# Kernel optimization log

Hardware: AMD Instinct MI355X
Metric: run time of the kernel (lower is better)

Reference implementation:

```python
import jax, jax.numpy as jnp
import numpy as np

WINDOW = 32


def _dilate(mask, iters=5):
    # scipy binary_dilation with default cross structure, `iters` iterations
    m = mask.copy()
    for _ in range(iters):
        d = m.copy()
        d[1:, :] |= m[:-1, :]
        d[:-1, :] |= m[1:, :]
        d[:, 1:] |= m[:, :-1]
        d[:, :-1] |= m[:, 1:]
        m = d
    return m


def _label8(mask):
    # skimage measure.label, default 8-connectivity, via min-label propagation
    h, w = mask.shape
    lab = np.where(mask, np.arange(1, mask.size + 1, dtype=np.int64).reshape(h, w), 0)
    BIG = mask.size + 2
    while True:
        p = np.pad(np.where(mask, lab, BIG), 1, constant_values=BIG)
        m = np.full((h, w), BIG, dtype=np.int64)
        for dy in (-1, 0, 1):
            for dx in (-1, 0, 1):
                m = np.minimum(m, p[1 + dy:1 + dy + h, 1 + dx:1 + dx + w])
        new = np.where(mask, m, 0)
        if np.array_equal(new, lab):
            break
        lab = new
    u = np.unique(lab)
    out = np.searchsorted(u, lab)
    if u[0] != 0:
        out = out + 1
    return out


def _malis(seg_flat, e1, e2, costs, pos):
    # MALIS edge weights: Kruskal on descending affinities with union-find;
    # pos=True counts same-(nonzero)-label pairs merged by each edge,
    # pos=False counts cross-label pairs between labeled nodes.
    n = seg_flat.size
    parent = np.arange(n)
    cnt = [dict() for _ in range(n)]
    for i in range(n):
        s = int(seg_flat[i])
        if s != 0:
            cnt[i][s] = 1
    w = np.zeros(costs.shape[0], np.float32)

    def find(x):
        r = x
        while parent[r] != r:
            r = parent[r]
        while parent[x] != r:
            parent[x], x = r, parent[x]
        return r

    order = np.argsort(-costs, kind='stable')
    for ei in order:
        ra, rb = find(int(e1[ei])), find(int(e2[ei]))
        if ra == rb:
            continue
        ca, cb = cnt[ra], cnt[rb]
        small, large = (ca, cb) if len(ca) <= len(cb) else (cb, ca)
        same = 0
        for kk, v in small.items():
            same += v * large.get(kk, 0)
        if pos:
            w[ei] = same
        else:
            sa = sum(ca.values())
            sb = sum(cb.values())
            w[ei] = sa * sb - same
        parent[rb] = ra
        for kk, v in cb.items():
            ca[kk] = ca.get(kk, 0) + v
        cnt[rb] = None
    return w


def compute_malis_weights(pred_np, target_np):
    B, C, H, W = pred_np.shape
    wn_full = np.zeros(pred_np.shape, np.float32)
    wp_full = np.zeros(pred_np.shape, np.float32)
    win = WINDOW
    idx = np.arange(win * win).reshape(win, win)
    e1 = np.concatenate([idx[:, :-1].ravel(), idx[:-1, :].ravel()])
    e2 = np.concatenate([idx[:, 1:].ravel(), idx[1:, :].ravel()])
    for k in range(H // win):
        for j in range(W // win):
            p = pred_np[:, :, k * win:(k + 1) * win, j * win:(j + 1) * win]
            t = target_np[:, :, k * win:(k + 1) * win, j * win:(j + 1) * win]
            costs = np.concatenate([
                (p[:, :, :, :-1] + p[:, :, :, 1:]).reshape(B, -1),
                (p[:, :, :-1, :] + p[:, :, 1:, :]).reshape(B, -1)], axis=1).astype(np.float32)
            gtc = np.concatenate([
                (t[:, :, :, :-1] + t[:, :, :, 1:]).reshape(B, -1),
                (t[:, :, :-1, :] + t[:, :, 1:, :]).reshape(B, -1)], axis=1).astype(np.float32)
            costs_n = costs.copy()
            costs_p = costs.copy()
            costs_n[gtc > 20] = 20
            costs_p[gtc < 10] = 0
            gtc = np.minimum(gtc, 20)
            for i in range(B):
                sg = _label8(_dilate(t[i, 0] == 0, 5) == 0)
                en = _malis(sg.ravel(), e1, e2, costs_n[i], False)
                ep = _malis(sg.ravel(), e1, e2, costs_p[i], True)
                sn = en.sum()
                if sn > 0:
                    en = en / sn
                sp = ep.sum()
                if sp > 0:
                    ep = ep / sp
                en[gtc[i] >= 10] = 0
                ep[gtc[i] < 20] = 0
                for ew, out in ((en, wn_full), (ep, wp_full)):
                    wh, wv = np.split(ew, 2)
                    wh = wh.reshape(win, win - 1)
                    wv = wv.reshape(win - 1, win)
                    nodes = np.zeros((win, win), np.float32)
                    nodes[:, :-1] += wh
                    nodes[:, 1:] += wh
                    nodes[:-1, :] += wv
                    nodes[1:, :] += wv
                    out[i, 0, k * win:(k + 1) * win, j * win:(j + 1) * win] = nodes
    return wn_full, wp_full


def setup_inputs() -> dict:
    key = jax.random.key(0)
    k1, k2 = jax.random.split(key)
    pred = jax.random.uniform(k1, (2, 1, 256, 256), jnp.float32) * 20.0
    target = jax.random.randint(k2, (2, 1, 256, 256), 0, 26).astype(jnp.float32)
    return {"pred": pred, "target": target, "malis_lr": 1.0, "malis_lr_pos": 1.0}


def reference(pred, target, malis_lr, malis_lr_pos):
    # weights are computed from detached values (CPU graph algorithm), constants wrt autodiff
    wn, wp = compute_malis_weights(np.asarray(pred), np.asarray(target))
    wn = jnp.asarray(wn, jnp.float32)
    wp = jnp.asarray(wp, jnp.float32)
    loss = malis_lr * jnp.square(pred) * wn + malis_lr_pos * jnp.square(20.0 - pred) * wp
    return loss.sum()
```

## Files before the change

### kernel.cpp

```cpp
#include <hip/hip_runtime.h>
#include <cstdint>

#define NPIX  1024
#define NH    992
#define NEDGE 1984
#define NSORT 2048
#define NGRP  31
#define HFS   4300
#define POOLN (NPIX + 2*HFS)

typedef unsigned long long u64;
typedef unsigned int u32;

static __device__ __forceinline__ u64 packRoot(int sL,int off,int len,int cap){
    return (u64)(u32)(sL & 0x7FF) | ((u64)(u32)(off & 0x3FFF) << 11) |
           ((u64)(u32)(len & 0x7FF) << 25) | ((u64)(u32)(cap & 0x7FF) << 36);
}
#define R_SL(R)  ((int)((R) & 0x7FF))
#define R_OFF(R) ((int)(((R)>>11) & 0x3FFF))
#define R_LEN(R) ((int)(((R)>>25) & 0x7FF))
#define R_CAP(R) ((int)(((R)>>36) & 0x7FF))
#define EMASK 0x3FFFFFFu

static __device__ __forceinline__ int rdl(int v, int l){ return __builtin_amdgcn_readlane(v, l); }

static __device__ __forceinline__ u64 sxor64(u64 v, int m){
    u32 lo = (u32)__shfl_xor((int)(v & 0xFFFFFFFFull), m, 64);
    u32 hi = (u32)__shfl_xor((int)(v >> 32), m, 64);
    return ((u64)hi << 32) | lo;
}

static __device__ __forceinline__ void edgeAB(int e, int &a, int &b){
    if (e < NH) { int r = (int)((unsigned)e / 31u); a = e + r; b = a + 1; }
    else        { a = e - NH; b = a + 32; }
}

#define CE(x, y, up) { u64 _a=(x), _b=(y); bool _lt=(_a<_b); \
    u64 _mn=_lt?_a:_b, _mx=_lt?_b:_a; (x)=(up)?_mn:_mx; (y)=(up)?_mx:_mn; }
#define CEX(x, xm, keepmin) { u64 _p=sxor64((x),(xm)); bool _lt=((x)<_p); \
    u64 _mn=_lt?(x):_p, _mx=_lt?_p:(x); (x)=(keepmin)?_mn:_mx; }

static __device__ __forceinline__ int wredi(int v){
    #pragma unroll
    for (int o = 32; o > 0; o >>= 1) v += __shfl_xor(v, o, 64);
    return v;
}
static __device__ __forceinline__ float wredf(float v){
    #pragma unroll
    for (int o = 32; o > 0; o >>= 1) v += __shfl_xor(v, o, 64);
    return v;
}

__global__ __launch_bounds__(128) void malis_kernel(
    const float* __restrict__ pred,
    const float* __restrict__ target,
    const float* __restrict__ lr_p,
    const float* __restrict__ lrp_p,
    float* __restrict__ out)
{
    const int tid  = threadIdx.x;
    const int lane = tid & 63;
    const int wv   = tid >> 6;
    const int bid  = blockIdx.x;
    const int bb   = bid >> 6;
    const int win  = bid & 63;
    const int wy   = win >> 3, wx = win & 7;
    const int base = bb * 65536 + (wy * 32) * 256 + wx * 32;

    __shared__ __align__(16) u32 Ks[2][NSORT];
    __shared__ u64   root[2][NPIX];
    __shared__ float predL[NPIX];
    __shared__ float costs[NEDGE];
    __shared__ u32   poolS[2][POOLN];
    __shared__ u32   Q[2][NPIX];
    __shared__ float Qw[2][NPIX];
    __shared__ short seg[NPIX];
    __shared__ short par[2][NPIX];
    __shared__ short H[2][NPIX + 1];
    __shared__ unsigned char tgtL[NPIX];
    __shared__ unsigned char gtcL[NEDGE];
    __shared__ u32   rowmaskL[32];
    __shared__ u32   fgL[32];
    __shared__ unsigned short baseL[33];
    __shared__ int   flags[2];

    u32* runPar = (u32*)poolS;
    unsigned short* labIdRun = (unsigned short*)(runPar + 512);

    for (int j = 0; j < 8; ++j) {
        int i = tid + 128 * j;
        int r = i >> 5, c = i & 31;
        float pv = pred[base + r * 256 + c];
        float tv = target[base + r * 256 + c];
        predL[i] = pv;
        tgtL[i]  = (unsigned char)tv;
        u64 zb = __ballot(tv == 0.0f);
        if (lane == 0) {
            int rr = 4 * j + 2 * wv;
            rowmaskL[rr]     = (u32)zb;
            rowmaskL[rr + 1] = (u32)(zb >> 32);
        }
    }
    if (tid == 0) flags[1] = 0;
    for (int x = tid; x < 512; x += 128) runPar[x] = (u32)x;
    __syncthreads();

    if (tid < 32) {
        u32 m = rowmaskL[tid];
        #pragma unroll
        for (int it = 0; it < 5; ++it) {
            u32 um = __shfl(m, (tid == 0) ? 0 : tid - 1, 64);
            if (tid == 0) um = 0;
            u32 dm = __shfl(m, (tid == 31) ? 31 : tid + 1, 64);
            if (tid == 31) dm = 0;
            m = m | (m << 1) | (m >> 1) | um | dm;
        }
        u32 f = ~m;
        fgL[tid] = f;
        int ns = __popc(f & ~(f << 1));
        int x = ns;
        #pragma unroll
        for (int off = 1; off < 32; off <<= 1) {
            int y = __shfl(x, (tid >= off) ? tid - off : 0, 64);
            if (tid >= off) x += y;
        }
        baseL[tid] = (unsigned short)(x - ns);
        if (tid == 31) baseL[32] = (unsigned short)x;
    }
    __syncthreads();
    const int nRuns = (int)baseL[32];

    for (;;) {
        if (tid == 0) flags[0] = 0;
        __syncthreads();
        bool chg = false;
        for (int j = 0; j < 8; ++j) {
            int i = tid + 128 * j;
            int r = i >> 5, c = i & 31;
            if (r == 0) continue;
            u32 fr = fgL[r];
            if (!((fr >> c) & 1u)) continue;
            u32 fu = fgL[r - 1];
            u32 nb = fu & (u32)((7ull << c) >> 1);
            if (!nb) continue;
            u32 Sr = fr & ~(fr << 1);
            int a = (int)baseL[r] + __popc(Sr & ((2u << c) - 1u)) - 1;
            for (;;) { int p = (int)runPar[a]; if (p == a) break; a = p; }
            u32 Su = fu & ~(fu << 1);
            int bu = (int)baseL[r - 1];
            while (nb) {
                int cc = __ffs((int)nb) - 1; nb &= nb - 1;
                int b = bu + __popc(Su & ((2u << cc) - 1u)) - 1;
                for (;;) { int p = (int)runPar[b]; if (p == b) break; b = p; }
                if (a != b) {
                    int mnr = a < b ? a : b;
                    int mxr = a ^ b ^ mnr;
                    atomicMin(&runPar[mxr], (u32)mnr);
                    chg = true;
                    a = mnr;
                }
            }
        }
        if (chg) flags[0] = 1;
        __syncthreads();
        if (!flags[0]) break;
        for (int x = tid; x < nRuns; x += 128) {
            u32 p = runPar[x];
            runPar[x] = runPar[p];
        }
        __syncthreads();
    }

    for (int x = tid; x < nRuns; x += 128)
        if ((int)runPar[x] == x) labIdRun[x] = (unsigned short)atomicAdd(&flags[1], 1);
    __syncthreads();

    for (int j = 0; j < 8; ++j) {
        int i = tid + 128 * j;
        int r = i >> 5, c = i & 31;
        u32 fr = fgL[r];
        short s = 0;
        if ((fr >> c) & 1u) {
            u32 Sr = fr & ~(fr << 1);
            int x = (int)baseL[r] + __popc(Sr & ((2u << c) - 1u)) - 1;
            for (;;) { int p = (int)runPar[x]; if (p == x) break; x = p; }
            s = (short)((int)labIdRun[x] + 1);
        }
        seg[i] = s;
    }

    for (int e = tid; e < NEDGE; e += 128) {
        int a, b2; edgeAB(e, a, b2);
        costs[e] = predL[a] + predL[b2];
        gtcL[e]  = (unsigned char)(tgtL[a] + tgtL[b2]);
    }
    __syncthreads();

    const int ph = wv;
    u32*   Ks_   = Ks[ph];
    short* par_  = par[ph];
    u64*   root_ = root[ph];
    u32*   pool_ = poolS[ph];
    short* H_    = H[ph];
    u32*   Q_    = Q[ph];
    float* Qw_   = Qw[ph];
    u32*   claim_= (u32*)Qw[ph];

    u64 sk[32];
    #pragma unroll
    for (int r = 0; r < 32; ++r) {
        int e = lane * 32 + r;
        u64 kv = ~0ULL;
        if (e < NEDGE) {
            float cv = costs[e];
            int g = gtcL[e];
            if (ph == 0) { if (g > 20) cv = 20.0f; }
            else         { if (g < 10) cv = 0.0f; }
            kv = (((u64)(~__float_as_uint(cv))) << 32) | (u32)e;
        }
        sk[r] = kv;
    }
    #pragma unroll
    for (int kk2 = 2; kk2 <= 32; kk2 <<= 1) {
        #pragma unroll
        for (int j = kk2 >> 1; j > 0; j >>= 1) {
            #pragma unroll
            for (int r = 0; r < 32; ++r) {
                if ((r & j) == 0) {
                    bool up = (kk2 == 32) ? ((lane & 1) == 0) : ((r & kk2) == 0);
                    CE(sk[r], sk[r | j], up);
                }
            }
        }
    }
    #pragma unroll
    for (int kk2 = 64; kk2 <= 2048; kk2 <<= 1) {
        const bool up = ((lane & (kk2 >> 5)) == 0);
        #pragma unroll
        for (int j = kk2 >> 1; j >= 32; j >>= 1) {
            const int xm = j >> 5;
            const bool keepmin = (((lane & xm) == 0) == up);
            #pragma unroll
            for (int r = 0; r < 32; ++r) { CEX(sk[r], xm, keepmin); }
        }
        #pragma unroll
        for (int j = 16; j > 0; j >>= 1) {
            #pragma unroll
            for (int r = 0; r < 32; ++r) {
                if ((r & j) == 0) { CE(sk[r], sk[r | j], up); }
            }
        }
    }
    #pragma unroll
    for (int r = 0; r < 32; r += 4) {
        uint4 v4;
        v4.x = (u32)sk[r]; v4.y = (u32)sk[r+1]; v4.z = (u32)sk[r+2]; v4.w = (u32)sk[r+3];
        *(uint4*)&Ks_[lane * 32 + r] = v4;
    }

    for (int i = lane; i < NPIX; i += 64) {
        short s2 = seg[i];
        par_[i] = (short)(i | (s2 ? 0x8000 : 0));
        root_[i] = s2 ? ((1ull << 62) | ((u32)(unsigned short)s2 << 16) | 1u) : 0ull;
        H_[i] = 0;
        claim_[i] = ~0u;
    }
    if (lane == 0) H_[NPIX] = 0;
    __builtin_amdgcn_wave_barrier();

    int qn = 0;
    u32 rnd = 1;
    const u64 ltm = (1ull << lane) - 1;
    int curE = (int)Ks_[lane];
    for (int g2 = 0; g2 < NGRP; ++g2) {
        int nextE = (g2 + 1 < NGRP) ? (int)Ks_[(g2 + 1) * 64 + lane] : 0;
        const int myE = curE;
        int ea, eb2; edgeAB(myE, ea, eb2);
        int ra = ea, rb = eb2;
        int laA, laB;
        for (;;) {
            int va = (int)(unsigned short)par_[ra];
            int vb = (int)(unsigned short)par_[rb];
            int pa = va & 0x3FF, pb = vb & 0x3FF;
            bool fa = (pa != ra), fb = (pb != rb);
            if (!fa && !fb) { laA = va >> 15; laB = vb >> 15; break; }
            int ga = (int)(unsigned short)par_[pa];
            int gb = (int)(unsigned short)par_[pb];
            if (fa) { par_[ra] = (short)ga; ra = ga & 0x3FF; }
            if (fb) { par_[rb] = (short)gb; rb = gb & 0x3FF; }
        }
        bool alive = (ra != rb);

        for (;;) {
            if (!__ballot(alive)) break;
            const bool av = alive;
            const u32 tag = ((0x03FFFFFFu - rnd) << 6) | (u32)lane;
            ++rnd;
            int mn = ra < rb ? ra : rb;
            int mx = ra < rb ? rb : ra;
            int winner = (laA == laB) ? mn : (laA ? ra : rb);
            int loser  = (laA == laB) ? mx : (laA ? rb : ra);
            bool wgt = (laA & laB) != 0;
            if (av)        atomicMin(&claim_[loser],  tag);
            if (av && wgt) atomicMin(&claim_[winner], tag);
            bool sel = false;
            if (av) {
                u32 cl = claim_[loser];
                u32 cw = wgt ? claim_[winner] : tag;
                sel = (cl == tag) && (cw == tag);
            }
            u64 wm = __ballot(sel && wgt);
            if (sel && wgt) Q_[qn + __popcll(wm & ltm)] =
                (u32)myE | ((u32)mn << 11) | ((u32)mx << 21);
            qn += (int)__popcll(wm);
            if (sel) par_[loser] = (short)winner;
            if (av) {
                for (;;) {
                    int va = (int)(unsigned short)par_[ra];
                    int vb = (int)(unsigned short)par_[rb];
                    int pa = va & 0x3FF, pb = vb & 0x3FF;
                    bool fa = (pa != ra), fb = (pb != rb);
                    if (!fa && !fb) { laA = va >> 15; laB = vb >> 15; break; }
                    int ga = (int)(unsigned short)par_[pa];
                    int gb = (int)(unsigned short)par_[pb];
                    if (fa) { par_[ra] = (short)ga; ra = ga & 0x3FF; }
                    if (fb) { par_[rb] = (short)gb; rb = gb & 0x3FF; }
                }
                alive = !sel && (ra != rb);
            }
        }
        curE = nextE;
        __builtin_amdgcn_wave_barrier();
    }

    u32 bump = NPIX;
    u32 halfEnd = NPIX + HFS;
    int curHalf = 0;

    auto do_gc = [&]() {
        u32 tgt = (curHalf == 0) ? (u32)(NPIX + HFS) : (u32)NPIX;
        u32 nb = tgt;
        for (int c = 0; c < 16; ++c) {
            int i0 = c * 64 + lane;
            u64 Ri = root_[i0];
            bool live = (Ri != 0) && ((Ri >> 62) == 0);
            u64 rbm = __ballot(live);
            while (rbm) {
                int j = __ffsll(rbm) - 1; rbm &= rbm - 1;
                int r = c * 64 + j;
                u64 R = root_[r];
                int len = R_LEN(R);
                int off = R_OFF(R);
                for (int t = lane; t < len; t += 64) {
                    u32 v2 = pool_[off + t];
                    pool_[nb + t] = v2;
                }
                __builtin_amdgcn_wave_barrier();
                if (lane == 0) root_[r] = packRoot(R_SL(R), (int)nb, len, len);
                nb += (u32)len;
            }
        }
        bump = nb;
        halfEnd = tgt + HFS;
        curHalf ^= 1;
    };

    u32 rec = 0; u64 RA = 0, RB = 0;
    if (qn > 0) {
        rec = Q_[0];
        int A0 = (int)((rec >> 11) & 0x3FF), B0 = (int)((rec >> 21) & 0x3FF);
        RA = root_[A0]; RB = root_[B0];
    }
    for (int q = 0; q < qn; ++q) {
        const int A = (int)((rec >> 11) & 0x3FF);
        const int B = (int)((rec >> 21) & 0x3FF);
        int tA = (int)(RA >> 62), tB = (int)(RB >> 62);
        int same, sLa, sLb;
        u64 newR;

        if (tA == 1 && tB == 1) {
            u32 pa = (u32)RA & EMASK, pb = (u32)RB & EMASK;
            int ca = (int)(pa & 0xFFFF), cb = (int)(pb & 0xFFFF);
            sLa = ca; sLb = cb;
            if ((pa >> 16) == (pb >> 16)) {
                same = ca * cb;
                newR = (1ull << 62) | (u64)(pa + (u32)cb);
            } else {
                same = 0;
                newR = (2ull << 62) | ((u64)pb << 26) | pa;
            }
        } else {
            int lenA = tA ? tA : R_LEN(RA);
            int lenB = tB ? tB : R_LEN(RB);
            if (bump + (u32)(lenA + lenB + 8) > halfEnd) {
                do_gc();
                RA = root_[A]; RB = root_[B];
                tA = (int)(RA >> 62); tB = (int)(RB >> 62);
                lenA = tA ? tA : R_LEN(RA);
                lenB = tB ? tB : R_LEN(RB);
            }
            int offA = 0, capA = 0, offB = 0, capB = 0;
            if (tA == 0) { sLa = R_SL(RA); offA = R_OFF(RA); capA = R_CAP(RA); }
            else {
                u32 a0 = (u32)RA & EMASK, a1 = (u32)(RA >> 26) & EMASK;
                sLa = (int)(a0 & 0xFFFF) + ((tA == 2) ? (int)(a1 & 0xFFFF) : 0);
            }
            if (tB == 0) { sLb = R_SL(RB); offB = R_OFF(RB); capB = R_CAP(RB); }
            else {
                u32 b0 = (u32)RB & EMASK, b1 = (u32)(RB >> 26) & EMASK;
                sLb = (int)(b0 & 0xFFFF) + ((tB == 2) ? (int)(b1 & 0xFFFF) : 0);
            }
            u32 eA = 0, eB = 0;
            if (lenA <= 64) {
                if (tA == 0) { if (lane < lenA) eA = pool_[offA + lane]; }
                else {
                    u32 a0 = (u32)RA & EMASK, a1 = (u32)(RA >> 26) & EMASK;
                    eA = (lane == 0) ? a0 : ((lane == 1 && tA == 2) ? a1 : 0);
                }
            }
            if (lenB <= 64) {
                if (tB == 0) { if (lane < lenB) eB = pool_[offB + lane]; }
                else {
                    u32 b0 = (u32)RB & EMASK, b1 = (u32)(RB >> 26) & EMASK;
                    eB = (lane == 0) ? b0 : ((lane == 1 && tB == 2) ? b1 : 0);
                }
            }
            u32 eS, eL; int lenS, lenL, offS, offL, capL, tS, tL;
            if (lenA <= lenB) { eS=eA; lenS=lenA; offS=offA; tS=tA; eL=eB; lenL=lenB; offL=offB; capL=capB; tL=tB; }
            else              { eS=eB; lenS=lenB; offS=offB; tS=tB; eL=eA; lenL=lenA; offL=offA; capL=capA; tL=tA; }
            int dOff, dLen, dCap;
            same = 0;

            if (lenS + lenL <= 64) {
                dLen = lenL;
                for (int t = 0; t < lenS; ++t) {
                    u32 xs = (u32)rdl((int)eS, t);
                    bool match = (lane < lenL) && ((eL >> 16) == (xs >> 16));
                    u64 mb = __ballot(match);
                    if (mb) {
                        int ml = __ffsll(mb) - 1;
                        same += (int)(xs & 0xFFFF) * ((int)rdl((int)eL, ml) & 0xFFFF);
                        if (match) eL += (xs & 0xFFFF);
                    } else {
                        if (lane == dLen) eL = xs;
                        dLen++;
                    }
                }
                if (dLen <= 2) {
                    u32 m0 = (u32)rdl((int)eL, 0) & EMASK;
                    u32 m1 = (dLen > 1) ? ((u32)rdl((int)eL, 1) & EMASK) : 0u;
                    newR = ((u64)(u32)dLen << 62) | ((u64)m1 << 26) | m0;
                } else {
                    if (tL == 0 && dLen <= capL) { dOff = offL; dCap = capL; }
                    else { dOff = (int)bump; dCap = (dLen + 3) & ~3; bump += (u32)dCap; }
                    if (lane < dLen) pool_[dOff + lane] = eL;
                    newR = packRoot(sLa + sLb, dOff, dLen, dCap);
                }
            } else {
                dOff = (int)bump;
                dCap = (lenL + lenS + 4) & ~3; bump += (u32)dCap;
                if (lenS <= 64) {
                    if (lane < lenS) H_[eS >> 16] = (short)(eS & 0xFFFF);
                } else {
                    for (int j = lane; j < lenS; j += 64) {
                        u32 es = pool_[offS + j];
                        H_[es >> 16] = (short)(es & 0xFFFF);
                    }
                }
                __builtin_amdgcn_wave_barrier();
                int sp = 0;
                for (int j = lane; j < lenL; j += 64) {
                    u32 el = pool_[offL + j];
                    int h = (int)H_[el >> 16];
                    sp += h * (int)(el & 0xFFFF);
                    pool_[dOff + j] = el + (u32)h;
                    if (h) H_[el >> 16] = 0;
                }
                same = wredi(sp);
                __builtin_amdgcn_wave_barrier();
                int baseU = 0;
                if (lenS <= 64) {
                    bool un = (lane < lenS) && (H_[eS >> 16] != 0);
                    u64 ub = __ballot(un);
                    if (un) {
                        int pos = __popcll(ub & ltm);
                        pool_[dOff + lenL + pos] = eS;
                        H_[eS >> 16] = 0;
                    }
                    baseU = (int)__popcll(ub);
                } else {
                    for (int j0 = 0; j0 < lenS; j0 += 64) {
                        int j = j0 + lane;
                        bool un = false; u32 es = 0;
                        if (j < lenS) { es = pool_[offS + j]; un = (H_[es >> 16] != 0); }
                        u64 ub = __ballot(un);
                        if (un) {
                            int pos = __popcll(ub & ltm);
                            pool_[dOff + lenL + baseU + pos] = es;
                            H_[es >> 16] = 0;
                        }
                        baseU += (int)__popcll(ub);
                    }
                }
                dLen = lenL + baseU;
                newR = packRoot(sLa + sLb, dOff, dLen, dCap);
            }
        }

        float w = (float)(ph ? same : (sLa * sLb - same));

        u32 recN = 0; int An = -1, Bn = -1; u64 RAn = 0, RBn = 0;
        if (q + 1 < qn) {
            recN = Q_[q + 1];
            An = (int)((recN >> 11) & 0x3FF);
            Bn = (int)((recN >> 21) & 0x3FF);
            RAn = root_[An]; RBn = root_[Bn];
        }
        if (lane == 0) {
            Qw_[q] = w;
            root_[A] = newR;
            root_[B] = 0;
        }
        __builtin_amdgcn_wave_barrier();
        if (An == A) RAn = newR;
        if (Bn == A) RBn = newR;
        rec = recN; RA = RAn; RB = RBn;
    }

    float s_loc = 0.0f;
    for (int q = lane; q < qn; q += 64) s_loc += Qw_[q];
    const float sn = wredf(s_loc);

    const float scale = ph ? lrp_p[0] : lr_p[0];
    float acc = 0.0f;
    for (int q = lane; q < qn; q += 64) {
        float wv2 = Qw_[q];
        if (wv2 == 0.0f) continue;
        if (sn > 0.0f) wv2 /= sn;
        int me = (int)(Q_[q] & 0x7FF);
        int g = gtcL[me];
        bool zero = ph ? (g < 20) : (g >= 10);
        if (zero) continue;
        int a2, b2; edgeAB(me, a2, b2);
        float pa = predL[a2], pb = predL[b2];
        float fa2, fb2;
        if (ph == 0) { fa2 = pa * pa; fb2 = pb * pb; }
        else { float qa = 20.0f - pa, qb = 20.0f - pb; fa2 = qa * qa; fb2 = qb * qb; }
        acc += scale * wv2 * (fa2 + fb2);
    }
    acc = wredf(acc);
    if (lane == 0) atomicAdd(out, acc);
}

__global__ void zero_out_kernel(float* o)
{
    if (threadIdx.x == 0 && blockIdx.x == 0) o[0] = 0.0f;
}

extern "C" void kernel_launch(void* const* d_in, const int* in_sizes, int n_in,
                              void* d_out, int out_size, void* d_ws, size_t ws_size,
                              hipStream_t stream)
{
    const float* pred   = (const float*)d_in[0];
    const float* target = (const float*)d_in[1];
    const float* lr     = (const float*)d_in[2];
    const float* lrp    = (const float*)d_in[3];
    float* out = (float*)d_out;

    zero_out_kernel<<<1, 64, 0, stream>>>(out);
    malis_kernel<<<128, 128, 0, stream>>>(pred, target, lr, lrp, out);
}
```

Before: 337.2 us.

## Fuse label-histogram merging into the parallel union-find rounds

Folds the serial per-merge label-count processing into the wave-parallel Kruskal claim loop. Each lane whose merge involves small inline roots (one or two labels) computes its weight and updates the roots itself. Only merges that overflow fall back to a serialized per-lane pool path inside the loop. This removes the separate sequential replay over the merge queue, at the cost of a dedicated claim array, more shared memory, and extra divergence and register pressure in the hot loop.

```diff
diff --git a/kernel.cpp b/kernel.cpp
--- a/kernel.cpp
+++ b/kernel.cpp
@@ -72,8 +72,9 @@
     __shared__ float predL[NPIX];
     __shared__ float costs[NEDGE];
     __shared__ u32   poolS[2][POOLN];
-    __shared__ u32   Q[2][NPIX];
+    __shared__ unsigned short Q[2][NPIX];
     __shared__ float Qw[2][NPIX];
+    __shared__ u32   claimS[2][NPIX];
     __shared__ short seg[NPIX];
     __shared__ short par[2][NPIX];
     __shared__ short H[2][NPIX + 1];
@@ -202,9 +203,9 @@
     u64*   root_ = root[ph];
     u32*   pool_ = poolS[ph];
     short* H_    = H[ph];
-    u32*   Q_    = Q[ph];
+    unsigned short* Q_ = Q[ph];
     float* Qw_   = Qw[ph];
-    u32*   claim_= (u32*)Qw[ph];
+    u32*   claim_= claimS[ph];
 
     u64 sk[32];
     #pragma unroll
@@ -268,9 +269,41 @@
     if (lane == 0) H_[NPIX] = 0;
     __builtin_amdgcn_wave_barrier();
 
+    const u64 ltm = (1ull << lane) - 1;
+    u32 bump = NPIX;
+    u32 halfEnd = NPIX + HFS;
+    int curHalf = 0;
+
+    auto do_gc = [&]() {
+        u32 tgt = (curHalf == 0) ? (u32)(NPIX + HFS) : (u32)NPIX;
+        u32 nb = tgt;
+        for (int c = 0; c < 16; ++c) {
+            int i0 = c * 64 + lane;
+            u64 Ri = root_[i0];
+            bool live = (Ri != 0) && ((Ri >> 62) == 0);
+            u64 rbm = __ballot(live);
+            while (rbm) {
+                int j = __ffsll(rbm) - 1; rbm &= rbm - 1;
+                int r = c * 64 + j;
+                u64 R = root_[r];
+                int len = R_LEN(R);
+                int off = R_OFF(R);
+                for (int t = lane; t < len; t += 64) {
+                    u32 v2 = pool_[off + t];
+                    pool_[nb + t] = v2;
+                }
+                __builtin_amdgcn_wave_barrier();
+                if (lane == 0) root_[r] = packRoot(R_SL(R), (int)nb, len, len);
+                nb += (u32)len;
+            }
+        }
+        bump = nb;
+        halfEnd = tgt + HFS;
+        curHalf ^= 1;
+    };
+
     int qn = 0;
     u32 rnd = 1;
-    const u64 ltm = (1ull << lane) - 1;
     int curE = (int)Ks_[lane];
     for (int g2 = 0; g2 < NGRP; ++g2) {
         int nextE = (g2 + 1 < NGRP) ? (int)Ks_[(g2 + 1) * 64 + lane] : 0;
@@ -297,7 +330,7 @@
             const u32 tag = ((0x03FFFFFFu - rnd) << 6) | (u32)lane;
             ++rnd;
             int mn = ra < rb ? ra : rb;
-            int mx = ra < rb ? rb : ra;
+            int mx = ra ^ rb ^ mn;
             int winner = (laA == laB) ? mn : (laA ? ra : rb);
             int loser  = (laA == laB) ? mx : (laA ? rb : ra);
             bool wgt = (laA & laB) != 0;
@@ -310,10 +343,182 @@
                 sel = (cl == tag) && (cw == tag);
             }
             u64 wm = __ballot(sel && wgt);
-            if (sel && wgt) Q_[qn + __popcll(wm & ltm)] =
-                (u32)myE | ((u32)mn << 11) | ((u32)mx << 21);
+            int qidx = qn + (int)__popcll(wm & ltm);
             qn += (int)__popcll(wm);
             if (sel) par_[loser] = (short)winner;
+
+            bool needPool = false;
+            if (sel && wgt) {
+                u64 RW = root_[mn], RL = root_[mx];
+                int tW = (int)(RW >> 62), tL2 = (int)(RL >> 62);
+                if (tW != 0 && tL2 != 0) {
+                    u32 a0 = (u32)RW & EMASK, a1 = (u32)(RW >> 26) & EMASK;
+                    u32 b0 = (u32)RL & EMASK, b1 = (u32)(RL >> 26) & EMASK;
+                    u32 la0 = a0 >> 16, la1 = a1 >> 16;
+                    u32 lb0 = b0 >> 16, lb1 = b1 >> 16;
+                    int ca0 = (int)(a0 & 0xFFFF), ca1 = (int)(a1 & 0xFFFF);
+                    int cb0 = (int)(b0 & 0xFFFF), cb1 = (int)(b1 & 0xFFFF);
+                    int sLa = ca0 + ((tW == 2) ? ca1 : 0);
+                    int sLb = cb0 + ((tL2 == 2) ? cb1 : 0);
+                    int same = 0;
+                    if (lb0 == la0) same += ca0 * cb0;
+                    else if (tW == 2 && lb0 == la1) same += ca1 * cb0;
+                    if (tL2 == 2) {
+                        if (lb1 == la0) same += ca0 * cb1;
+                        else if (tW == 2 && lb1 == la1) same += ca1 * cb1;
+                    }
+                    u32 r0 = a0, r1 = (tW == 2) ? a1 : 0;
+                    int n = tW; bool ovf = false;
+                    if (lb0 == la0) r0 += (u32)cb0;
+                    else if (tW == 2 && lb0 == la1) r1 += (u32)cb0;
+                    else { if (n == 1) { r1 = b0; n = 2; } else ovf = true; }
+                    if (tL2 == 2) {
+                        if (lb1 == la0) r0 += (u32)cb1;
+                        else if (tW == 2 && lb1 == la1) r1 += (u32)cb1;
+                        else { if (n == 1) { r1 = b1; n = 2; } else ovf = true; }
+                    }
+                    if (!ovf) {
+                        root_[mn] = ((u64)(u32)n << 62) | ((u64)r1 << 26) | r0;
+                        root_[mx] = 0;
+                        Qw_[qidx] = (float)(ph ? same : (sLa * sLb - same));
+                        Q_[qidx]  = (unsigned short)myE;
+                    } else needPool = true;
+                } else needPool = true;
+            }
+
+            u64 pm = __ballot(needPool);
+            while (pm) {
+                int f = __ffsll(pm) - 1; pm &= pm - 1;
+                int A  = rdl(mn, f),  B  = rdl(mx, f);
+                int e  = rdl(myE, f), qi = rdl(qidx, f);
+                u64 RA = root_[A], RB = root_[B];
+                int tA = (int)(RA >> 62), tB = (int)(RB >> 62);
+                int lenA = tA ? tA : R_LEN(RA);
+                int lenB = tB ? tB : R_LEN(RB);
+                if (bump + (u32)(lenA + lenB + 8) > halfEnd) {
+                    do_gc();
+                    RA = root_[A]; RB = root_[B];
+                    tA = (int)(RA >> 62); tB = (int)(RB >> 62);
+                    lenA = tA ? tA : R_LEN(RA);
+                    lenB = tB ? tB : R_LEN(RB);
+                }
+                int sLa, sLb;
+                int offA = 0, capA = 0, offB = 0, capB = 0;
+                if (tA == 0) { sLa = R_SL(RA); offA = R_OFF(RA); capA = R_CAP(RA); }
+                else {
+                    u32 a0 = (u32)RA & EMASK, a1 = (u32)(RA >> 26) & EMASK;
+                    sLa = (int)(a0 & 0xFFFF) + ((tA == 2) ? (int)(a1 & 0xFFFF) : 0);
+                }
+                if (tB == 0) { sLb = R_SL(RB); offB = R_OFF(RB); capB = R_CAP(RB); }
+                else {
+                    u32 b0 = (u32)RB & EMASK, b1 = (u32)(RB >> 26) & EMASK;
+                    sLb = (int)(b0 & 0xFFFF) + ((tB == 2) ? (int)(b1 & 0xFFFF) : 0);
+                }
+                u32 eA = 0, eB = 0;
+                if (lenA <= 64) {
+                    if (tA == 0) { if (lane < lenA) eA = pool_[offA + lane]; }
+                    else {
+                        u32 a0 = (u32)RA & EMASK, a1 = (u32)(RA >> 26) & EMASK;
+                        eA = (lane == 0) ? a0 : ((lane == 1 && tA == 2) ? a1 : 0);
+                    }
+                }
+                if (lenB <= 64) {
+                    if (tB == 0) { if (lane < lenB) eB = pool_[offB + lane]; }
+                    else {
+                        u32 b0 = (u32)RB & EMASK, b1 = (u32)(RB >> 26) & EMASK;
+                        eB = (lane == 0) ? b0 : ((lane == 1 && tB == 2) ? b1 : 0);
+                    }
+                }
+                u32 eS, eL; int lenS, lenL, offS, offL, capL, tL;
+                if (lenA <= lenB) { eS=eA; lenS=lenA; offS=offA; eL=eB; lenL=lenB; offL=offB; capL=capB; tL=tB; }
+                else              { eS=eB; lenS=lenB; offS=offB; eL=eA; lenL=lenA; offL=offA; capL=capA; tL=tA; }
+                int dOff, dLen, dCap;
+                int same = 0;
+                u64 newR;
+
+                if (lenS + lenL <= 64) {
+                    dLen = lenL;
+                    for (int t = 0; t < lenS; ++t) {
+                        u32 xs = (u32)rdl((int)eS, t);
+                        bool match = (lane < lenL) && ((eL >> 16) == (xs >> 16));
+                        u64 mb = __ballot(match);
+                        if (mb) {
+                            int ml = __ffsll(mb) - 1;
+                            same += (int)(xs & 0xFFFF) * ((int)rdl((int)eL, ml) & 0xFFFF);
+                            if (match) eL += (xs & 0xFFFF);
+                        } else {
+                            if (lane == dLen) eL = xs;
+                            dLen++;
+                        }
+                    }
+                    if (dLen <= 2) {
+                        u32 m0 = (u32)rdl((int)eL, 0) & EMASK;
+                        u32 m1 = (dLen > 1) ? ((u32)rdl((int)eL, 1) & EMASK) : 0u;
+                        newR = ((u64)(u32)dLen << 62) | ((u64)m1 << 26) | m0;
+                    } else {
+                        if (tL == 0 && dLen <= capL) { dOff = offL; dCap = capL; }
+                        else { dOff = (int)bump; dCap = (dLen + 3) & ~3; bump += (u32)dCap; }
+                        if (lane < dLen) pool_[dOff + lane] = eL;
+                        newR = packRoot(sLa + sLb, dOff, dLen, dCap);
+                    }
+                } else {
+                    dOff = (int)bump;
+                    dCap = (lenL + lenS + 4) & ~3; bump += (u32)dCap;
+                    if (lenS <= 64) {
+                        if (lane < lenS) H_[eS >> 16] = (short)(eS & 0xFFFF);
+                    } else {
+                        for (int j = lane; j < lenS; j += 64) {
+                            u32 es = pool_[offS + j];
+                            H_[es >> 16] = (short)(es & 0xFFFF);
+                        }
+                    }
+                    __builtin_amdgcn_wave_barrier();
+                    int sp = 0;
+                    for (int j = lane; j < lenL; j += 64) {
+                        u32 el = pool_[offL + j];
+                        int h = (int)H_[el >> 16];
+                        sp += h * (int)(el & 0xFFFF);
+                        pool_[dOff + j] = el + (u32)h;
+                        if (h) H_[el >> 16] = 0;
+                    }
+                    same = wredi(sp);
+                    __builtin_amdgcn_wave_barrier();
+                    int baseU = 0;
+                    if (lenS <= 64) {
+                        bool un = (lane < lenS) && (H_[eS >> 16] != 0);
+                        u64 ub = __ballot(un);
+                        if (un) {
+                            int pos = __popcll(ub & ltm);
+                            pool_[dOff + lenL + pos] = eS;
+                            H_[eS >> 16] = 0;
+                        }
+                        baseU = (int)__popcll(ub);
+                    } else {
+                        for (int j0 = 0; j0 < lenS; j0 += 64) {
+                            int j = j0 + lane;
+                            bool un = false; u32 es = 0;
+                            if (j < lenS) { es = pool_[offS + j]; un = (H_[es >> 16] != 0); }
+                            u64 ub = __ballot(un);
+                            if (un) {
+                                int pos = __popcll(ub & ltm);
+                                pool_[dOff + lenL + baseU + pos] = es;
+                                H_[es >> 16] = 0;
+                            }
+                            baseU += (int)__popcll(ub);
+                        }
+                    }
+                    dLen = lenL + baseU;
+                    newR = packRoot(sLa + sLb, dOff, dLen, dCap);
+                }
+                if (lane == 0) {
+                    Qw_[qi] = (float)(ph ? same : (sLa * sLb - same));
+                    Q_[qi]  = (unsigned short)e;
+                    root_[A] = newR;
+                    root_[B] = 0;
+                }
+                __builtin_amdgcn_wave_barrier();
+            }
+
             if (av) {
                 for (;;) {
                     int va = (int)(unsigned short)par_[ra];
@@ -333,200 +538,6 @@
         __builtin_amdgcn_wave_barrier();
     }
 
-    u32 bump = NPIX;
-    u32 halfEnd = NPIX + HFS;
-    int curHalf = 0;
-
-    auto do_gc = [&]() {
-        u32 tgt = (curHalf == 0) ? (u32)(NPIX + HFS) : (u32)NPIX;
-        u32 nb = tgt;
-        for (int c = 0; c < 16; ++c) {
-            int i0 = c * 64 + lane;
-            u64 Ri = root_[i0];
-            bool live = (Ri != 0) && ((Ri >> 62) == 0);
-            u64 rbm = __ballot(live);
-            while (rbm) {
-                int j = __ffsll(rbm) - 1; rbm &= rbm - 1;
-                int r = c * 64 + j;
-                u64 R = root_[r];
-                int len = R_LEN(R);
-                int off = R_OFF(R);
-                for (int t = lane; t < len; t += 64) {
-                    u32 v2 = pool_[off + t];
-                    pool_[nb + t] = v2;
-                }
-                __builtin_amdgcn_wave_barrier();
-                if (lane == 0) root_[r] = packRoot(R_SL(R), (int)nb, len, len);
-                nb += (u32)len;
-            }
-        }
-        bump = nb;
-        halfEnd = tgt + HFS;
-        curHalf ^= 1;
-    };
-
-    u32 rec = 0; u64 RA = 0, RB = 0;
-    if (qn > 0) {
-        rec = Q_[0];
-        int A0 = (int)((rec >> 11) & 0x3FF), B0 = (int)((rec >> 21) & 0x3FF);
-        RA = root_[A0]; RB = root_[B0];
-    }
-    for (int q = 0; q < qn; ++q) {
-        const int A = (int)((rec >> 11) & 0x3FF);
-        const int B = (int)((rec >> 21) & 0x3FF);
-        int tA = (int)(RA >> 62), tB = (int)(RB >> 62);
-        int same, sLa, sLb;
-        u64 newR;
-
-        if (tA == 1 && tB == 1) {
-            u32 pa = (u32)RA & EMASK, pb = (u32)RB & EMASK;
-            int ca = (int)(pa & 0xFFFF), cb = (int)(pb & 0xFFFF);
-            sLa = ca; sLb = cb;
-            if ((pa >> 16) == (pb >> 16)) {
-                same = ca * cb;
-                newR = (1ull << 62) | (u64)(pa + (u32)cb);
-            } else {
-                same = 0;
-                newR = (2ull << 62) | ((u64)pb << 26) | pa;
-            }
-        } else {
-            int lenA = tA ? tA : R_LEN(RA);
-            int lenB = tB ? tB : R_LEN(RB);
-            if (bump + (u32)(lenA + lenB + 8) > halfEnd) {
-                do_gc();
-                RA = root_[A]; RB = root_[B];
-                tA = (int)(RA >> 62); tB = (int)(RB >> 62);
-                lenA = tA ? tA : R_LEN(RA);
-                lenB = tB ? tB : R_LEN(RB);
-            }
-            int offA = 0, capA = 0, offB = 0, capB = 0;
-            if (tA == 0) { sLa = R_SL(RA); offA = R_OFF(RA); capA = R_CAP(RA); }
-            else {
-                u32 a0 = (u32)RA & EMASK, a1 = (u32)(RA >> 26) & EMASK;
-                sLa = (int)(a0 & 0xFFFF) + ((tA == 2) ? (int)(a1 & 0xFFFF) : 0);
-            }
-            if (tB == 0) { sLb = R_SL(RB); offB = R_OFF(RB); capB = R_CAP(RB); }
-            else {
-                u32 b0 = (u32)RB & EMASK, b1 = (u32)(RB >> 26) & EMASK;
-                sLb = (int)(b0 & 0xFFFF) + ((tB == 2) ? (int)(b1 & 0xFFFF) : 0);
-            }
-            u32 eA = 0, eB = 0;
-            if (lenA <= 64) {
-                if (tA == 0) { if (lane < lenA) eA = pool_[offA + lane]; }
-                else {
-                    u32 a0 = (u32)RA & EMASK, a1 = (u32)(RA >> 26) & EMASK;
-                    eA = (lane == 0) ? a0 : ((lane == 1 && tA == 2) ? a1 : 0);
-                }
-            }
-            if (lenB <= 64) {
-                if (tB == 0) { if (lane < lenB) eB = pool_[offB + lane]; }
-                else {
-                    u32 b0 = (u32)RB & EMASK, b1 = (u32)(RB >> 26) & EMASK;
-                    eB = (lane == 0) ? b0 : ((lane == 1 && tB == 2) ? b1 : 0);
-                }
-            }
-            u32 eS, eL; int lenS, lenL, offS, offL, capL, tS, tL;
-            if (lenA <= lenB) { eS=eA; lenS=lenA; offS=offA; tS=tA; eL=eB; lenL=lenB; offL=offB; capL=capB; tL=tB; }
-            else              { eS=eB; lenS=lenB; offS=offB; tS=tB; eL=eA; lenL=lenA; offL=offA; capL=capA; tL=tA; }
-            int dOff, dLen, dCap;
-            same = 0;
-
-            if (lenS + lenL <= 64) {
-                dLen = lenL;
-                for (int t = 0; t < lenS; ++t) {
-                    u32 xs = (u32)rdl((int)eS, t);
-                    bool match = (lane < lenL) && ((eL >> 16) == (xs >> 16));
-                    u64 mb = __ballot(match);
-                    if (mb) {
-                        int ml = __ffsll(mb) - 1;
-                        same += (int)(xs & 0xFFFF) * ((int)rdl((int)eL, ml) & 0xFFFF);
-                        if (match) eL += (xs & 0xFFFF);
-                    } else {
-                        if (lane == dLen) eL = xs;
-                        dLen++;
-                    }
-                }
-                if (dLen <= 2) {
-                    u32 m0 = (u32)rdl((int)eL, 0) & EMASK;
-                    u32 m1 = (dLen > 1) ? ((u32)rdl((int)eL, 1) & EMASK) : 0u;
-                    newR = ((u64)(u32)dLen << 62) | ((u64)m1 << 26) | m0;
-                } else {
-                    if (tL == 0 && dLen <= capL) { dOff = offL; dCap = capL; }
-                    else { dOff = (int)bump; dCap = (dLen + 3) & ~3; bump += (u32)dCap; }
-                    if (lane < dLen) pool_[dOff + lane] = eL;
-                    newR = packRoot(sLa + sLb, dOff, dLen, dCap);
-                }
-            } else {
-                dOff = (int)bump;
-                dCap = (lenL + lenS + 4) & ~3; bump += (u32)dCap;
-                if (lenS <= 64) {
-                    if (lane < lenS) H_[eS >> 16] = (short)(eS & 0xFFFF);
-                } else {
-                    for (int j = lane; j < lenS; j += 64) {
-                        u32 es = pool_[offS + j];
-                        H_[es >> 16] = (short)(es & 0xFFFF);
-                    }
-                }
-                __builtin_amdgcn_wave_barrier();
-                int sp = 0;
-                for (int j = lane; j < lenL; j += 64) {
-                    u32 el = pool_[offL + j];
-                    int h = (int)H_[el >> 16];
-                    sp += h * (int)(el & 0xFFFF);
-                    pool_[dOff + j] = el + (u32)h;
-                    if (h) H_[el >> 16] = 0;
-                }
-                same = wredi(sp);
-                __builtin_amdgcn_wave_barrier();
-                int baseU = 0;
-                if (lenS <= 64) {
-                    bool un = (lane < lenS) && (H_[eS >> 16] != 0);
-                    u64 ub = __ballot(un);
-                    if (un) {
-                        int pos = __popcll(ub & ltm);
-                        pool_[dOff + lenL + pos] = eS;
-                        H_[eS >> 16] = 0;
-                    }
-                    baseU = (int)__popcll(ub);
-                } else {
-                    for (int j0 = 0; j0 < lenS; j0 += 64) {
-                        int j = j0 + lane;
-                        bool un = false; u32 es = 0;
-                        if (j < lenS) { es = pool_[offS + j]; un = (H_[es >> 16] != 0); }
-                        u64 ub = __ballot(un);
-                        if (un) {
-                            int pos = __popcll(ub & ltm);
-                            pool_[dOff + lenL + baseU + pos] = es;
-                            H_[es >> 16] = 0;
-                        }
-                        baseU += (int)__popcll(ub);
-                    }
-                }
-                dLen = lenL + baseU;
-                newR = packRoot(sLa + sLb, dOff, dLen, dCap);
-            }
-        }
-
-        float w = (float)(ph ? same : (sLa * sLb - same));
-
-        u32 recN = 0; int An = -1, Bn = -1; u64 RAn = 0, RBn = 0;
-        if (q + 1 < qn) {
-            recN = Q_[q + 1];
-            An = (int)((recN >> 11) & 0x3FF);
-            Bn = (int)((recN >> 21) & 0x3FF);
-            RAn = root_[An]; RBn = root_[Bn];
-        }
-        if (lane == 0) {
-            Qw_[q] = w;
-            root_[A] = newR;
-            root_[B] = 0;
-        }
-        __builtin_amdgcn_wave_barrier();
-        if (An == A) RAn = newR;
-        if (Bn == A) RBn = newR;
-        rec = recN; RA = RAn; RB = RBn;
-    }
-
     float s_loc = 0.0f;
     for (int q = lane; q < qn; q += 64) s_loc += Qw_[q];
     const float sn = wredf(s_loc);
@@ -537,7 +548,7 @@
         float wv2 = Qw_[q];
         if (wv2 == 0.0f) continue;
         if (sn > 0.0f) wv2 /= sn;
-        int me = (int)(Q_[q] & 0x7FF);
+        int me = (int)Q_[q];
         int g = gtcL[me];
         bool zero = ph ? (g < 20) : (g >= 10);
         if (zero) continue;
```

New measurement: 322.4 us. -4.4%, faster.
